# Performance work log

Measured on AMD Instinct MI355X. Metric: run time of the kernel, lower is better.

## Reference

```python
import jax, jax.numpy as jnp
import numpy as np

PART = 0  # index of '<PART>' tag in vocab (select_part_tag = zeros)
W = 3     # max_word_len


def lstm_scan(x_seq, h0, c0, Wih, Whh, bih, bhh):
    """x_seq: [S, N, D] -> outputs [S, N, H]. torch LSTM gate order i, f, g, o."""
    def cell(carry, x):
        h, c = carry
        g = x @ Wih.T + bih + h @ Whh.T + bhh
        i, f, gg, o = jnp.split(g, 4, axis=-1)
        c = jax.nn.sigmoid(f) * c + jax.nn.sigmoid(i) * jnp.tanh(gg)
        h = jax.nn.sigmoid(o) * jnp.tanh(c)
        return (h, c), h
    _, hs = jax.lax.scan(cell, (h0, c0), x_seq)
    return hs


def decoder_probs(win, h0, emb, Wih, Whh, bih, bhh, Wp, bp):
    """Decoder.forward for all start positions at once.
    win: [N, W] candidate-word tokens; h0: [N, H] (used as both h0 and c0).
    Returns [W, N]: row y = log p(word win[:, :y+1] then <PART>)."""
    N = win.shape[0]
    toks = jnp.concatenate([jnp.full((N, 1), PART, win.dtype), win], axis=1)  # prepend <PART>
    x = jnp.swapaxes(emb[toks], 0, 1)                    # [W+1, N, D]
    hs = lstm_scan(x, h0, h0, Wih, Whh, bih, bhh)        # [W+1, N, H]
    logits = hs @ Wp.T + bp                              # [W+1, N, V]
    logZ = jax.nn.logsumexp(logits, axis=-1)             # [W+1, N]
    # log_softmax gathered at target char / <PART> tag positions
    char = jnp.take_along_axis(logits[:-1], win.T[:, :, None], axis=-1)[..., 0] - logZ[:-1]  # [W, N]
    tag = logits[1:, :, PART] - logZ[1:]                 # [W, N]
    return jnp.cumsum(char, axis=0) + tag                # cumulative char logprob + end tag


def forward_loss(sentence, emb, enc, decf, decb):
    B, T = sentence.shape
    H = enc[1].shape[1]
    fvec = sentence
    bvec = jnp.flip(sentence, axis=1)

    def encode(vec):
        toks = jnp.concatenate([jnp.full((B, 1), PART, vec.dtype), vec[:, :-1]], axis=1)
        x = jnp.swapaxes(emb[toks], 0, 1)                # [T, B, D]
        z = jnp.zeros((B, H), emb.dtype)
        return lstm_scan(x, z, z, *enc)                  # [T, B, H]

    enc_f, enc_b = encode(fvec), encode(bvec)
    idx = jnp.clip(jnp.arange(T)[:, None] + jnp.arange(W)[None, :], 0, T - 1)  # [T, W]

    def run_dec(vec, enc_out, params):
        win = vec[:, idx].reshape(B * T, W)              # window starting at each position
        h0 = jnp.swapaxes(enc_out, 0, 1).reshape(B * T, -1)
        p = decoder_probs(win, h0, emb, *params)         # [W, B*T]
        return p.reshape(W, B, T).transpose(2, 0, 1)     # [T(start), W(len-1), B]

    fwdP = run_dec(fvec, enc_f, decf)
    bwdP = run_dec(bvec, enc_b, decb)

    xs = jnp.arange(T)[:, None]
    ys = jnp.arange(W)[None, :]
    # SGB_A.add_bidirection: P[x, y, b] = score of word of length y+1 ending at position x
    P = 0.5 * (fwdP[jnp.clip(xs - ys, 0, T - 1), ys] + bwdP[T - 1 - xs, ys])  # [T, W, B]

    # compute_all_probability: semi-CRF forward recursion
    NEG = jnp.asarray(-1e30, P.dtype)
    def step(buf, inp):
        # buf[i] = total[j-1-i]
        p_j, j = inp
        cand = jnp.where((jnp.arange(W) < j)[:, None], buf + p_j, NEG)
        tot = jax.nn.logsumexp(cand, axis=0)
        return jnp.concatenate([tot[None], buf[:-1]], axis=0), tot

    _, totals = jax.lax.scan(step, jnp.zeros((W, B), P.dtype), (P, jnp.arange(1, T + 1)))
    return -jnp.mean(totals[-1])


def setup_inputs() -> dict:
    key = jax.random.key(0)
    V, D, H, B, T = 8000, 256, 256, 16, 128
    ks = jax.random.split(key, 24)
    s_d = 1.0 / np.sqrt(D)
    s_h = 1.0 / np.sqrt(H)

    def mat(k, shape, scale):
        return jax.random.normal(k, shape, jnp.float32) * scale

    def lstm_p(k):
        k1, k2, k3, k4 = jax.random.split(k, 4)
        return (mat(k1, (4 * H, D), s_d), mat(k2, (4 * H, H), s_h),
                mat(k3, (4 * H,), s_h), mat(k4, (4 * H,), s_h))

    enc = lstm_p(ks[1])
    decf_l = lstm_p(ks[2])
    decb_l = lstm_p(ks[3])
    inp = {
        "sentence": jax.random.randint(ks[0], (B, T), 0, V, jnp.int32),
        "emb": mat(ks[4], (V, D), 1.0),
        "enc_Wih": enc[0], "enc_Whh": enc[1], "enc_bih": enc[2], "enc_bhh": enc[3],
        "decf_Wih": decf_l[0], "decf_Whh": decf_l[1], "decf_bih": decf_l[2], "decf_bhh": decf_l[3],
        "decf_Wp": mat(ks[5], (V, H), s_h), "decf_bp": mat(ks[6], (V,), s_h),
        "decb_Wih": decb_l[0], "decb_Whh": decb_l[1], "decb_bih": decb_l[2], "decb_bhh": decb_l[3],
        "decb_Wp": mat(ks[7], (V, H), s_h), "decb_bp": mat(ks[8], (V,), s_h),
    }
    return inp


def reference(sentence, emb, enc_Wih, enc_Whh, enc_bih, enc_bhh,
              decf_Wih, decf_Whh, decf_bih, decf_bhh, decf_Wp, decf_bp,
              decb_Wih, decb_Whh, decb_bih, decb_bhh, decb_Wp, decb_bp):
    return forward_loss(
        sentence, emb,
        (enc_Wih, enc_Whh, enc_bih, enc_bhh),
        (decf_Wih, decf_Whh, decf_bih, decf_bhh, decf_Wp, decf_bp),
        (decb_Wih, decb_Whh, decb_bih, decb_bhh, decb_Wp, decb_bp))
```

## Files before the change

### kernel.cpp

```cpp
#include <hip/hip_runtime.h>
#include <math.h>

#define VOCAB 8000
#define NN 2048

typedef unsigned short u16;
typedef __attribute__((ext_vector_type(8))) short short8v;
typedef __attribute__((ext_vector_type(4))) short short4v;
typedef __attribute__((ext_vector_type(4))) float float4v;
typedef __attribute__((ext_vector_type(4))) int int4v;

#define OFF_WPBF   0ul
#define OFF_WDEC   2048000ul
#define OFF_XENC   2572288ul
#define OFF_H0BF   4153344ul
#define OFF_DECX   4677632ul
#define OFF_CDEC   6250496ul
#define OFF_HSBF   7299072ul
#define OFF_GBUF   9396224ul
#define OFF_LOGZ   13590528ul
#define OFF_GCH    13606912ul
#define OFF_GTG    13619200ul
#define OFF_P      13631488ul
#define OFF_WTOK   13637632ul
#define OFF_XP0    13649920ul
#define OFF_ENCW   13652032ul
#define OFF_SENC   13914240ul
#define OFF_SQ     13915264ul
#define OFF_WQI8   13916288ul

__device__ __forceinline__ float sigf(float x) { return 1.0f / (1.0f + __expf(-x)); }
__device__ __forceinline__ float tanhsafe(float x) {
    x = fminf(15.0f, fmaxf(-15.0f, x));
    float e = __expf(2.0f * x);
    return (e - 1.0f) / (e + 1.0f);
}
__device__ __forceinline__ u16 f2bf(float f) {
    union { float f; unsigned int u; } x; x.f = f;
    return (u16)((x.u + 0x7fffu + ((x.u >> 16) & 1u)) >> 16);
}
__device__ __forceinline__ float bf2f(u16 x) {
    union { unsigned int u; float f; } v; v.u = ((unsigned int)x) << 16;
    return v.f;
}

__device__ __forceinline__ short8v ldfrag(const u16* lds, int row, int k, int lane, int SB) {
    int r = row + (lane & 15);
    int off = r * SB + ((k + ((lane >> 4) << 3)) << 1);
    off ^= (r & 7) << 4;
    return *(const short8v*)((const char*)lds + off);
}

__device__ __forceinline__ void stage128x256(const u16* __restrict__ g, int row0, int rowmax,
                                             int rowstride, int col0, u16* lds, int tid) {
    #pragma unroll
    for (int it = 0; it < 16; ++it) {
        int chunk = tid + it * 256;
        int r = chunk >> 5;
        int kc = (chunk & 31) << 3;
        short8v v = {0, 0, 0, 0, 0, 0, 0, 0};
        if (row0 + r < rowmax)
            v = *(const short8v*)(g + (size_t)(row0 + r) * rowstride + col0 + kc);
        int off = (r * 512 + kc * 2) ^ ((r & 7) << 4);
        *(short8v*)((char*)lds + off) = v;
    }
}


__global__ __launch_bounds__(256) void k_wpbf(const float* __restrict__ Wf,
                                              const float* __restrict__ Wb,
                                              u16* __restrict__ out) {
    int chunk = blockIdx.x * 256 + threadIdx.x;
    int kc = (chunk & 31) << 3;
    int v = (chunk >> 5) % 8000;
    int d = chunk / (8000 * 32);
    const float* src = (d ? Wb : Wf) + (size_t)v * 256 + kc;
    u16 t8[8];
    #pragma unroll
    for (int j = 0; j < 8; ++j) t8[j] = f2bf(src[j]);
    *(short8v*)(out + ((size_t)d * 8000 + v) * 256 + kc) = *(short8v*)t8;
}

__global__ __launch_bounds__(256) void k_wdecbf(const float* __restrict__ fWhh, const float* __restrict__ fWih,
                                                const float* __restrict__ bWhh, const float* __restrict__ bWih,
                                                u16* __restrict__ out) {
    int chunk = blockIdx.x * 256 + threadIdx.x;
    int kc = (chunk & 63) << 3;
    int r = (chunk >> 6) & 1023;
    int d = chunk >> 16;
    const float* Whh = d ? bWhh : fWhh;
    const float* Wih = d ? bWih : fWih;
    const float* src = (kc < 256) ? (Whh + (size_t)r * 256 + kc) : (Wih + (size_t)r * 256 + (kc - 256));
    u16 t8[8];
    #pragma unroll
    for (int j = 0; j < 8; ++j) t8[j] = f2bf(src[j]);
    *(short8v*)(out + ((size_t)d * 1024 + r) * 512 + kc) = *(short8v*)t8;
}

__global__ __launch_bounds__(256) void k_wencbf(const float* __restrict__ Whh, const float* __restrict__ Wih,
                                                u16* __restrict__ out) {
    int chunk = blockIdx.x * 256 + threadIdx.x;
    int kc = (chunk & 63) << 3;
    int r = chunk >> 6;
    const float* src = (kc < 256) ? (Whh + (size_t)r * 256 + kc) : (Wih + (size_t)r * 256 + (kc - 256));
    u16 t8[8];
    #pragma unroll
    for (int j = 0; j < 8; ++j) t8[j] = f2bf(src[j]);
    *(short8v*)(out + (size_t)r * 512 + kc) = *(short8v*)t8;
}

__global__ __launch_bounds__(256) void k_escale(const float* __restrict__ Whh,
                                                float* __restrict__ s_enc,
                                                float* __restrict__ sq) {
    int r = blockIdx.x * 256 + threadIdx.x;
    if (r >= 1024) return;
    float m = 0.0f;
    for (int k = 0; k < 256; ++k) m = fmaxf(m, fabsf(Whh[r * 256 + k]));
    s_enc[r] = m / 16129.0f;
    sq[r] = (m > 0.0f) ? 127.0f / m : 0.0f;
}

__global__ __launch_bounds__(256) void k_wq2(const float* __restrict__ Whh,
                                             const float* __restrict__ sq,
                                             signed char* __restrict__ wq) {
    int lin = blockIdx.x * 256 + threadIdx.x;
    int lane = lin & 63;
    int ks = (lin >> 6) & 3;
    int c = (lin >> 8) & 3;
    int w = lin >> 10;
    int r = c * 256 + w * 16 + (lane & 15);
    int kb = ks * 64 + ((lane >> 4) << 4);
    float s = sq[r];
    signed char o16[16];
    #pragma unroll
    for (int j = 0; j < 16; ++j) {
        float q = rintf(Whh[r * 256 + kb + j] * s);
        q = fminf(127.0f, fmaxf(-127.0f, q));
        o16[j] = (signed char)q;
    }
    *(int4v*)(wq + (size_t)lin * 16) = *(int4v*)o16;
}

__global__ __launch_bounds__(256) void k_xenc(const int* __restrict__ S, const float* __restrict__ emb,
                                              u16* __restrict__ out) {
    int chunk = blockIdx.x * 256 + threadIdx.x;
    int kc = (chunk & 31) << 3;
    int b = (chunk >> 5) & 15;
    int t = (chunk >> 9) & 127;
    int d = chunk >> 16;
    int tok = 0;
    if (t > 0) tok = d ? S[b * 128 + 128 - t] : S[b * 128 + t - 1];
    const float* src = emb + (size_t)tok * 256 + kc;
    u16 t8[8];
    #pragma unroll
    for (int j = 0; j < 8; ++j) t8[j] = f2bf(src[j]);
    *(short8v*)(out + (size_t)(((d * 128 + t) * 16) + b) * 256 + kc) = *(short8v*)t8;
}

__global__ __launch_bounds__(256) void k_decx(const int* __restrict__ S, const float* __restrict__ emb,
                                              u16* __restrict__ decX, int* __restrict__ winTok) {
    int chunk = blockIdx.x * 256 + threadIdx.x;
    int kc = (chunk & 31) << 3;
    int n = (chunk >> 5) & 2047;
    int r2 = chunk >> 16;
    int s = r2 % 3, d = r2 / 3;
    int b = n >> 7, tq = n & 127;
    int pos = min(tq + s, 127);
    int tok = d ? S[b * 128 + 127 - pos] : S[b * 128 + pos];
    const float* src = emb + (size_t)tok * 256 + kc;
    u16 t8[8];
    #pragma unroll
    for (int j = 0; j < 8; ++j) t8[j] = f2bf(src[j]);
    *(short8v*)(decX + ((size_t)(d * 3 + s) * NN + n) * 256 + kc) = *(short8v*)t8;
    if ((chunk & 31) == 0) winTok[(d * 3 + s) * NN + n] = tok;
}

__global__ __launch_bounds__(256) void k_xp0(const float* __restrict__ emb,
                                             const float* __restrict__ Wihf,
                                             const float* __restrict__ Wihb,
                                             float* __restrict__ xp0) {
    int idx = blockIdx.x * 256 + threadIdx.x;
    int d = idx >> 10, r = idx & 1023;
    const float* Wih = d ? Wihb : Wihf;
    float acc = 0.0f;
    for (int k = 0; k < 256; ++k) acc = fmaf(emb[k], Wih[r * 256 + k], acc);
    xp0[idx] = acc;
}

__global__ __launch_bounds__(256) void k_xproj(const u16* __restrict__ xEncBF,
                                               const u16* __restrict__ encW,
                                               const float* __restrict__ ebih,
                                               const float* __restrict__ ebhh,
                                               float* __restrict__ xpT) {
    __shared__ u16 At[128 * 256];
    __shared__ u16 Bt[128 * 256];
    const int tid = threadIdx.x, lane = tid & 63, wid = tid >> 6;
    const int wm = wid >> 1, wv = wid & 1;
    const int r0 = blockIdx.x * 128, n0 = blockIdx.y * 128, d = blockIdx.z;
    stage128x256(xEncBF + (size_t)d * 2048 * 256, n0, 1 << 30, 256, 0, At, tid);
    stage128x256(encW, r0, 1 << 30, 512, 256, Bt, tid);
    __syncthreads();
    float4v acc[4][4];
    #pragma unroll
    for (int m = 0; m < 4; ++m)
        #pragma unroll
        for (int v = 0; v < 4; ++v) acc[m][v] = (float4v){0.f, 0.f, 0.f, 0.f};
    #pragma unroll
    for (int k = 0; k < 8; ++k) {
        short8v af[4], bf[4];
        #pragma unroll
        for (int m = 0; m < 4; ++m) af[m] = ldfrag(At, wm * 64 + m * 16, k * 32, lane, 512);
        #pragma unroll
        for (int v = 0; v < 4; ++v) bf[v] = ldfrag(Bt, wv * 64 + v * 16, k * 32, lane, 512);
        #pragma unroll
        for (int m = 0; m < 4; ++m)
            #pragma unroll
            for (int v = 0; v < 4; ++v)
                acc[m][v] = __builtin_amdgcn_mfma_f32_16x16x32_bf16(af[m], bf[v], acc[m][v], 0, 0, 0);
    }
    float bs[4]; int rg[4];
    #pragma unroll
    for (int v = 0; v < 4; ++v) {
        rg[v] = r0 + wv * 64 + v * 16 + (lane & 15);
        bs[v] = ebih[rg[v]] + ebhh[rg[v]];
    }
    #pragma unroll
    for (int m = 0; m < 4; ++m)
        #pragma unroll
        for (int i = 0; i < 4; ++i) {
            int n = n0 + wm * 64 + m * 16 + ((lane >> 4) << 2) + i;
            int t_ = n >> 4, bfull = n & 15;
            #pragma unroll
            for (int v = 0; v < 4; ++v) {
                int g = rg[v] >> 8, u = rg[v] & 255;
                size_t idx4 = (((size_t)(d * 16 + bfull) * 128 + t_) * 16 + (u >> 4)) * 16 + (u & 15);
                xpT[idx4 * 4 + g] = acc[m][v][i] + bs[v];
            }
        }
}

__global__ __launch_bounds__(1024) void k_enc5(const signed char* __restrict__ wq,
                                               const float* __restrict__ s_enc,
                                               const float4v* __restrict__ xpT4,
                                               u16* __restrict__ h0bf) {
    __shared__ signed char hbuf[2][4096];
    const int tid = threadIdx.x, lane = tid & 63, w = tid >> 6;
    const int blk = blockIdx.x, d = blk >> 4, b = blk & 15;
    const int l15 = lane & 15, hi = lane >> 4;
    int4v breg[4][4];
    #pragma unroll
    for (int c = 0; c < 4; ++c)
        #pragma unroll
        for (int ks = 0; ks < 4; ++ks)
            breg[c][ks] = *(const int4v*)(wq + ((size_t)(((w * 4 + c) * 4 + ks) * 64 + lane)) * 16);
    float sreg[4];
    #pragma unroll
    for (int c = 0; c < 4; ++c) sreg[c] = s_enc[c * 256 + w * 16 + l15];
    float creg = 0.0f;
    ((long*)hbuf)[tid] = 0l;
    const bool cellane = (lane < 16);
    const int u = w * 16 + l15;
    const float4v* xbase = xpT4 + ((size_t)(d * 16 + b) * 128) * 256 + w * 16 + l15;
    float4v xv_next = {0.f, 0.f, 0.f, 0.f};
    if (cellane) xv_next = xbase[0];
    __syncthreads();
    for (int t = 0; t < 128; ++t) {
        int cur = t & 1;
        float4v xv = xv_next;
        if (cellane && t < 127) xv_next = xbase[(size_t)(t + 1) * 256];
        int4v af[4];
        #pragma unroll
        for (int ks = 0; ks < 4; ++ks) {
            int off = (l15 * 256 + ks * 64 + hi * 16) ^ ((l15 & 7) << 4);
            af[ks] = *(const int4v*)(hbuf[cur] + off);
        }
        int4v acc[4];
        #pragma unroll
        for (int c = 0; c < 4; ++c) {
            acc[c] = (int4v){0, 0, 0, 0};
            #pragma unroll
            for (int ks = 0; ks < 4; ++ks)
                acc[c] = __builtin_amdgcn_mfma_i32_16x16x64_i8(af[ks], breg[c][ks], acc[c], 0, 0, 0);
        }
        if (cellane) {
            float gi = (float)acc[0][0] * sreg[0] + xv[0];
            float gf = (float)acc[1][0] * sreg[1] + xv[1];
            float gG = (float)acc[2][0] * sreg[2] + xv[2];
            float go = (float)acc[3][0] * sreg[3] + xv[3];
            float cn = sigf(gf) * creg + sigf(gi) * tanhsafe(gG);
            float h = sigf(go) * tanhsafe(cn);
            creg = cn;
            h0bf[((size_t)d * NN + b * 128 + t) * 256 + u] = f2bf(h);
            hbuf[cur ^ 1][u] = (signed char)rintf(h * 127.0f);
        }
        __syncthreads();
    }
}

__global__ __launch_bounds__(256) void k_decmm(const u16* __restrict__ Ah, size_t ahStride,
                                               const u16* __restrict__ Axx, size_t axStride,
                                               const u16* __restrict__ Wdec,
                                               const float* __restrict__ bihf, const float* __restrict__ bhhf,
                                               const float* __restrict__ bihb, const float* __restrict__ bhhb,
                                               const float* __restrict__ xp0, int useX,
                                               float* __restrict__ gBuf) {
    __shared__ u16 At[128 * 256];
    __shared__ u16 Bt[128 * 256];
    const int tid = threadIdx.x, lane = tid & 63, wid = tid >> 6;
    const int wm = wid >> 1, wv = wid & 1;
    const int r0 = blockIdx.x * 128, n0 = blockIdx.y * 128, d = blockIdx.z;
    float4v acc[4][4];
    #pragma unroll
    for (int m = 0; m < 4; ++m)
        #pragma unroll
        for (int v = 0; v < 4; ++v) acc[m][v] = (float4v){0.f, 0.f, 0.f, 0.f};
    const int nph = useX ? 2 : 1;
    for (int ph = 0; ph < nph; ++ph) {
        const u16* Asrc = (ph == 0) ? (Ah + (size_t)d * ahStride) : (Axx + (size_t)d * axStride);
        stage128x256(Asrc, n0, 1 << 30, 256, 0, At, tid);
        stage128x256(Wdec + (size_t)d * 1024 * 512, r0, 1 << 30, 512, ph * 256, Bt, tid);
        __syncthreads();
        #pragma unroll
        for (int k = 0; k < 8; ++k) {
            short8v af[4], bf[4];
            #pragma unroll
            for (int m = 0; m < 4; ++m) af[m] = ldfrag(At, wm * 64 + m * 16, k * 32, lane, 512);
            #pragma unroll
            for (int v = 0; v < 4; ++v) bf[v] = ldfrag(Bt, wv * 64 + v * 16, k * 32, lane, 512);
            #pragma unroll
            for (int m = 0; m < 4; ++m)
                #pragma unroll
                for (int v = 0; v < 4; ++v)
                    acc[m][v] = __builtin_amdgcn_mfma_f32_16x16x32_bf16(af[m], bf[v], acc[m][v], 0, 0, 0);
        }
        __syncthreads();
    }
    const float* bih = d ? bihb : bihf;
    const float* bhh = d ? bhhb : bhhf;
    float bs[4]; int rg[4];
    #pragma unroll
    for (int v = 0; v < 4; ++v) {
        rg[v] = r0 + wv * 64 + v * 16 + (lane & 15);
        bs[v] = bih[rg[v]] + bhh[rg[v]];
        if (!useX) bs[v] += xp0[d * 1024 + rg[v]];
    }
    #pragma unroll
    for (int m = 0; m < 4; ++m)
        #pragma unroll
        for (int i = 0; i < 4; ++i) {
            int n = n0 + wm * 64 + m * 16 + ((lane >> 4) << 2) + i;
            #pragma unroll
            for (int v = 0; v < 4; ++v)
                gBuf[((size_t)d * NN + n) * 1024 + rg[v]] = acc[m][v][i] + bs[v];
        }
}

__global__ __launch_bounds__(256) void k_deccell(const float* __restrict__ gBuf,
                                                 const u16* __restrict__ h0bf,
                                                 float* __restrict__ cDec,
                                                 u16* __restrict__ hsBF, int s) {
    int flat = blockIdx.x * 256 + threadIdx.x;
    int j = flat & 255;
    int n = (flat >> 8) & 2047;
    int d = flat >> 19;
    const float* g = gBuf + ((size_t)d * NN + n) * 1024;
    float gi = g[j], gf = g[j + 256], gg = g[j + 512], go = g[j + 768];
    float cprev = (s == 0) ? bf2f(h0bf[flat]) : cDec[flat];
    float cn = sigf(gf) * cprev + sigf(gi) * tanhsafe(gg);
    float h = sigf(go) * tanhsafe(cn);
    cDec[flat] = cn;
    hsBF[((size_t)(d * 4 + s) * NN + n) * 256 + j] = f2bf(h);
}

__global__ __launch_bounds__(512, 2) void k_proj8(const u16* __restrict__ hsBF,
                                                  const u16* __restrict__ WpBF,
                                                  const float* __restrict__ bpf, const float* __restrict__ bpb,
                                                  const int* __restrict__ winTok,
                                                  float* __restrict__ partials,
                                                  float* __restrict__ gchar, float* __restrict__ gtag) {
    __shared__ u16 At[128 * 256];
    __shared__ u16 Bt[2][64 * 256];
    const int tid = threadIdx.x, lane = tid & 63, w = tid >> 6;
    const int wm = w >> 1, wv = w & 1;
    const int l15 = lane & 15, hi = lane >> 4;
    const int L = blockIdx.x;
    const int chunkI = L & 7, idx = L >> 3;
    const int n0 = (idx & 15) * 128, d = idx >> 4;
    const int vt0 = chunkI * 16;
    const int nvt = min(16, 125 - vt0);
    const float* bp = d ? bpb : bpf;

#define LOADB8(vt_) do {                                                          \
        _Pragma("unroll")                                                         \
        for (int it = 0; it < 4; ++it) {                                          \
            int g = tid + it * 512; int r = g >> 5, kc = (g & 31) << 3;           \
            bregs[it] = *(const short8v*)(WpBF + ((size_t)d * 8000 + (vt_) * 64 + r) * 256 + kc); \
        }                                                                         \
    } while (0)
#define WRITEB8(buf_) do {                                                        \
        _Pragma("unroll")                                                         \
        for (int it = 0; it < 4; ++it) {                                          \
            int g = tid + it * 512; int r = g >> 5, kc = (g & 31) << 3;           \
            int off = (r * 512 + kc * 2) ^ ((r & 7) << 4);                        \
            *(short8v*)((char*)Bt[buf_] + off) = bregs[it];                       \
        }                                                                         \
    } while (0)

    short8v bregs[4];
    for (int s = 0; s < 4; ++s) {
        const u16* hsA = hsBF + (size_t)(d * 4 + s) * NN * 256;
        #pragma unroll
        for (int it = 0; it < 8; ++it) {
            int chunk = tid + it * 512;
            int r = chunk >> 5, kc = (chunk & 31) << 3;
            short8v v8 = *(const short8v*)(hsA + (size_t)(n0 + r) * 256 + kc);
            int off = (r * 512 + kc * 2) ^ ((r & 7) << 4);
            *(short8v*)((char*)At + off) = v8;
        }
        LOADB8(vt0);
        WRITEB8(0);
        int tok[2][4];
        #pragma unroll
        for (int m = 0; m < 2; ++m)
            #pragma unroll
            for (int i = 0; i < 4; ++i) {
                int n = n0 + wm * 32 + m * 16 + hi * 4 + i;
                tok[m][i] = (s < 3) ? winTok[(d * 3 + s) * NN + n] : -1;
            }
        float expsum[2][4] = {{0.f, 0.f, 0.f, 0.f}, {0.f, 0.f, 0.f, 0.f}};
        __syncthreads();
        short8v afr[2][8];
        #pragma unroll
        for (int m = 0; m < 2; ++m)
            #pragma unroll
            for (int kk = 0; kk < 8; ++kk) {
                afr[m][kk] = ldfrag(At, wm * 32 + m * 16, kk * 32, lane, 512);
                asm volatile("" : "+v"(afr[m][kk]));
            }
        int cur = 0;
        for (int t = 0; t < nvt; ++t) {
            int vt = vt0 + t;
            if (t + 1 < nvt) LOADB8(vt + 1);
            float bpv[2];
            #pragma unroll
            for (int v = 0; v < 2; ++v) bpv[v] = bp[vt * 64 + wv * 32 + v * 16 + l15];
            float4v acc[2][2];
            #pragma unroll
            for (int m = 0; m < 2; ++m)
                #pragma unroll
                for (int v = 0; v < 2; ++v) acc[m][v] = (float4v){0.f, 0.f, 0.f, 0.f};
            #pragma unroll
            for (int kk = 0; kk < 8; ++kk) {
                short8v bf[2];
                #pragma unroll
                for (int v = 0; v < 2; ++v) bf[v] = ldfrag(Bt[cur], wv * 32 + v * 16, kk * 32, lane, 512);
                #pragma unroll
                for (int m = 0; m < 2; ++m)
                    #pragma unroll
                    for (int v = 0; v < 2; ++v)
                        acc[m][v] = __builtin_amdgcn_mfma_f32_16x16x32_bf16(afr[m][kk], bf[v], acc[m][v], 0, 0, 0);
            }
            #pragma unroll
            for (int m = 0; m < 2; ++m)
                #pragma unroll
                for (int i = 0; i < 4; ++i) {
                    int n = n0 + wm * 32 + m * 16 + hi * 4 + i;
                    float es = 0.0f;
                    #pragma unroll
                    for (int v = 0; v < 2; ++v) {
                        int vgv = vt * 64 + wv * 32 + v * 16 + l15;
                        float lg = acc[m][v][i] + bpv[v];
                        es += __expf(lg);
                        if (vgv == tok[m][i]) gchar[(d * 3 + s) * NN + n] = lg;
                        if (s >= 1 && vgv == 0) gtag[(d * 3 + (s - 1)) * NN + n] = lg;
                    }
                    expsum[m][i] += es;
                }
            __syncthreads();
            if (t + 1 < nvt) WRITEB8(cur ^ 1);
            __syncthreads();
            cur ^= 1;
        }
        #pragma unroll
        for (int m = 0; m < 2; ++m)
            #pragma unroll
            for (int i = 0; i < 4; ++i) {
                float e = expsum[m][i];
                #pragma unroll
                for (int off = 1; off <= 8; off <<= 1) e += __shfl_xor(e, off);
                if (l15 == 0) {
                    int n = n0 + wm * 32 + m * 16 + hi * 4 + i;
                    partials[((size_t)(d * 4 + s) * NN + n) * 16 + chunkI * 2 + wv] = e;
                }
            }
    }
#undef LOADB8
#undef WRITEB8
}

__global__ __launch_bounds__(256) void k_lzsum(const float* __restrict__ partials,
                                               float* __restrict__ logZ) {
    int row = blockIdx.x * 256 + threadIdx.x;
    const float* p = partials + (size_t)row * 16;
    float s = 0.0f;
    #pragma unroll
    for (int c = 0; c < 16; ++c) s += p[c];
    logZ[row] = __logf(s);
}

__global__ __launch_bounds__(256) void k_passm(const float* __restrict__ gchar,
                                               const float* __restrict__ gtag,
                                               const float* __restrict__ logZ,
                                               float* __restrict__ P) {
    int flat = blockIdx.x * 256 + threadIdx.x;
    if (flat >= 128 * 3 * 16) return;
    int b = flat & 15;
    int y = (flat >> 4) % 3;
    int x = flat / 48;
    int nf = b * 128 + min(127, max(0, x - y));
    int nb = b * 128 + 127 - x;
    float pf = 0.0f, pb = 0.0f;
    for (int ss = 0; ss <= y; ++ss) {
        pf += gchar[ss * NN + nf] - logZ[ss * NN + nf];
        pb += gchar[(3 + ss) * NN + nb] - logZ[(4 + ss) * NN + nb];
    }
    pf += gtag[y * NN + nf] - logZ[(y + 1) * NN + nf];
    pb += gtag[(3 + y) * NN + nb] - logZ[(4 + y + 1) * NN + nb];
    P[flat] = 0.5f * (pf + pb);
}

__global__ __launch_bounds__(64) void k_scan(const float* __restrict__ P, float* __restrict__ out) {
    __shared__ float Pl[128 * 48];
    int tid = threadIdx.x;
    #pragma unroll
    for (int it = 0; it < 96; ++it) Pl[tid + it * 64] = P[tid + it * 64];
    __syncthreads();
    if (tid < 16) {
        int b = tid;
        float b0 = 0.f, b1 = 0.f, b2 = 0.f, tot = 0.f;
        for (int j = 1; j <= 128; ++j) {
            float c0 = b0 + Pl[((j - 1) * 3 + 0) * 16 + b];
            float c1 = (j >= 2) ? b1 + Pl[((j - 1) * 3 + 1) * 16 + b] : -1e30f;
            float c2 = (j >= 3) ? b2 + Pl[((j - 1) * 3 + 2) * 16 + b] : -1e30f;
            float mx = fmaxf(c0, fmaxf(c1, c2));
            float sv = __expf(c0 - mx) + __expf(c1 - mx) + __expf(c2 - mx);
            tot = mx + __logf(sv);
            b2 = b1; b1 = b0; b0 = tot;
        }
        #pragma unroll
        for (int off = 1; off <= 8; off <<= 1) tot += __shfl_xor(tot, off);
        if (b == 0) out[0] = -tot / 16.0f;
    }
}

extern "C" void kernel_launch(void* const* d_in, const int* in_sizes, int n_in,
                              void* d_out, int out_size, void* d_ws, size_t ws_size,
                              hipStream_t stream) {
    const int* S = (const int*)d_in[0];
    const float* emb = (const float*)d_in[1];
    const float* eWih = (const float*)d_in[2];
    const float* eWhh = (const float*)d_in[3];
    const float* ebih = (const float*)d_in[4];
    const float* ebhh = (const float*)d_in[5];
    const float* fWih = (const float*)d_in[6];
    const float* fWhh = (const float*)d_in[7];
    const float* fbih = (const float*)d_in[8];
    const float* fbhh = (const float*)d_in[9];
    const float* fWp  = (const float*)d_in[10];
    const float* fbp  = (const float*)d_in[11];
    const float* bWih = (const float*)d_in[12];
    const float* bWhh = (const float*)d_in[13];
    const float* bbih = (const float*)d_in[14];
    const float* bbhh = (const float*)d_in[15];
    const float* bWp  = (const float*)d_in[16];
    const float* bbp  = (const float*)d_in[17];

    float* w = (float*)d_ws;
    u16* WpBF    = (u16*)(w + OFF_WPBF);
    u16* WdecBF  = (u16*)(w + OFF_WDEC);
    u16* xEncBF  = (u16*)(w + OFF_XENC);
    u16* h0bf    = (u16*)(w + OFF_H0BF);
    u16* decXBF  = (u16*)(w + OFF_DECX);
    float* cDec  = w + OFF_CDEC;
    u16* hsBF    = (u16*)(w + OFF_HSBF);
    float* gBuf  = w + OFF_GBUF;
    float* xpT   = gBuf;
    float* partials = gBuf;
    float* logZ  = w + OFF_LOGZ;
    float* gchar = w + OFF_GCH;
    float* gtag  = w + OFF_GTG;
    float* Pm    = w + OFF_P;
    int* winTok  = (int*)(w + OFF_WTOK);
    float* xp0   = w + OFF_XP0;
    u16* encW    = (u16*)(w + OFF_ENCW);
    float* sEnc  = w + OFF_SENC;
    float* sQ    = w + OFF_SQ;
    signed char* wqEnc = (signed char*)(w + OFF_WQI8);

    k_wpbf<<<2000, 256, 0, stream>>>(fWp, bWp, WpBF);
    k_wdecbf<<<512, 256, 0, stream>>>(fWhh, fWih, bWhh, bWih, WdecBF);
    k_wencbf<<<256, 256, 0, stream>>>(eWhh, eWih, encW);
    k_escale<<<4, 256, 0, stream>>>(eWhh, sEnc, sQ);
    k_wq2<<<64, 256, 0, stream>>>(eWhh, sQ, wqEnc);
    k_xenc<<<512, 256, 0, stream>>>(S, emb, xEncBF);
    k_decx<<<1536, 256, 0, stream>>>(S, emb, decXBF, winTok);
    k_xp0<<<8, 256, 0, stream>>>(emb, fWih, bWih, xp0);

    k_xproj<<<dim3(8, 16, 2), 256, 0, stream>>>(xEncBF, encW, ebih, ebhh, xpT);
    k_enc5<<<32, 1024, 0, stream>>>(wqEnc, sEnc, (const float4v*)xpT, h0bf);

    for (int s = 0; s < 4; ++s) {
        const u16* Ah; size_t ahS;
        const u16* Axx; size_t axS;
        if (s == 0) {
            Ah = h0bf; ahS = (size_t)NN * 256;
            Axx = decXBF; axS = (size_t)3 * NN * 256;
        } else {
            Ah = hsBF + (size_t)(s - 1) * NN * 256; ahS = (size_t)4 * NN * 256;
            Axx = decXBF + (size_t)(s - 1) * NN * 256; axS = (size_t)3 * NN * 256;
        }
        k_decmm<<<dim3(8, 16, 2), 256, 0, stream>>>(Ah, ahS, Axx, axS, WdecBF,
                                                    fbih, fbhh, bbih, bbhh, xp0,
                                                    (s == 0) ? 0 : 1, gBuf);
        k_deccell<<<4096, 256, 0, stream>>>(gBuf, h0bf, cDec, hsBF, s);
    }

    k_proj8<<<256, 512, 0, stream>>>(hsBF, WpBF, fbp, bbp, winTok,
                                     partials, gchar, gtag);
    k_lzsum<<<64, 256, 0, stream>>>(partials, logZ);
    k_passm<<<24, 256, 0, stream>>>(gchar, gtag, logZ, Pm);
    k_scan<<<1, 64, 0, stream>>>(Pm, (float*)d_out);
}
```

Before: 492.6 us.

## Overlap decoder input projection with encoder recurrence and merge setup kernels

```diff
diff --git a/kernel.cpp b/kernel.cpp
--- a/kernel.cpp
+++ b/kernel.cpp
@@ -28,6 +28,8 @@
 #define OFF_SENC   13914240ul
 #define OFF_SQ     13915264ul
 #define OFF_WQI8   13916288ul
+#define OFF_GXD    13981824ul
+#define WS_NEED_OV ((OFF_GXD + 6291456ul) * 4ul)
 
 __device__ __forceinline__ float sigf(float x) { return 1.0f / (1.0f + __expf(-x)); }
 __device__ __forceinline__ float tanhsafe(float x) {
@@ -66,125 +68,110 @@
     }
 }
 
-
-__global__ __launch_bounds__(256) void k_wpbf(const float* __restrict__ Wf,
-                                              const float* __restrict__ Wb,
-                                              u16* __restrict__ out) {
-    int chunk = blockIdx.x * 256 + threadIdx.x;
-    int kc = (chunk & 31) << 3;
-    int v = (chunk >> 5) % 8000;
-    int d = chunk / (8000 * 32);
-    const float* src = (d ? Wb : Wf) + (size_t)v * 256 + kc;
-    u16 t8[8];
-    #pragma unroll
-    for (int j = 0; j < 8; ++j) t8[j] = f2bf(src[j]);
-    *(short8v*)(out + ((size_t)d * 8000 + v) * 256 + kc) = *(short8v*)t8;
-}
-
-__global__ __launch_bounds__(256) void k_wdecbf(const float* __restrict__ fWhh, const float* __restrict__ fWih,
-                                                const float* __restrict__ bWhh, const float* __restrict__ bWih,
-                                                u16* __restrict__ out) {
-    int chunk = blockIdx.x * 256 + threadIdx.x;
-    int kc = (chunk & 63) << 3;
-    int r = (chunk >> 6) & 1023;
-    int d = chunk >> 16;
-    const float* Whh = d ? bWhh : fWhh;
-    const float* Wih = d ? bWih : fWih;
-    const float* src = (kc < 256) ? (Whh + (size_t)r * 256 + kc) : (Wih + (size_t)r * 256 + (kc - 256));
-    u16 t8[8];
-    #pragma unroll
-    for (int j = 0; j < 8; ++j) t8[j] = f2bf(src[j]);
-    *(short8v*)(out + ((size_t)d * 1024 + r) * 512 + kc) = *(short8v*)t8;
-}
-
-__global__ __launch_bounds__(256) void k_wencbf(const float* __restrict__ Whh, const float* __restrict__ Wih,
-                                                u16* __restrict__ out) {
-    int chunk = blockIdx.x * 256 + threadIdx.x;
-    int kc = (chunk & 63) << 3;
-    int r = chunk >> 6;
-    const float* src = (kc < 256) ? (Whh + (size_t)r * 256 + kc) : (Wih + (size_t)r * 256 + (kc - 256));
-    u16 t8[8];
-    #pragma unroll
-    for (int j = 0; j < 8; ++j) t8[j] = f2bf(src[j]);
-    *(short8v*)(out + (size_t)r * 512 + kc) = *(short8v*)t8;
-}
-
-__global__ __launch_bounds__(256) void k_escale(const float* __restrict__ Whh,
-                                                float* __restrict__ s_enc,
-                                                float* __restrict__ sq) {
-    int r = blockIdx.x * 256 + threadIdx.x;
-    if (r >= 1024) return;
-    float m = 0.0f;
-    for (int k = 0; k < 256; ++k) m = fmaxf(m, fabsf(Whh[r * 256 + k]));
-    s_enc[r] = m / 16129.0f;
-    sq[r] = (m > 0.0f) ? 127.0f / m : 0.0f;
-}
-
-__global__ __launch_bounds__(256) void k_wq2(const float* __restrict__ Whh,
-                                             const float* __restrict__ sq,
-                                             signed char* __restrict__ wq) {
-    int lin = blockIdx.x * 256 + threadIdx.x;
-    int lane = lin & 63;
-    int ks = (lin >> 6) & 3;
-    int c = (lin >> 8) & 3;
-    int w = lin >> 10;
-    int r = c * 256 + w * 16 + (lane & 15);
-    int kb = ks * 64 + ((lane >> 4) << 4);
-    float s = sq[r];
-    signed char o16[16];
-    #pragma unroll
-    for (int j = 0; j < 16; ++j) {
-        float q = rintf(Whh[r * 256 + kb + j] * s);
-        q = fminf(127.0f, fmaxf(-127.0f, q));
-        o16[j] = (signed char)q;
-    }
-    *(int4v*)(wq + (size_t)lin * 16) = *(int4v*)o16;
-}
-
-__global__ __launch_bounds__(256) void k_xenc(const int* __restrict__ S, const float* __restrict__ emb,
-                                              u16* __restrict__ out) {
-    int chunk = blockIdx.x * 256 + threadIdx.x;
-    int kc = (chunk & 31) << 3;
-    int b = (chunk >> 5) & 15;
-    int t = (chunk >> 9) & 127;
-    int d = chunk >> 16;
-    int tok = 0;
-    if (t > 0) tok = d ? S[b * 128 + 128 - t] : S[b * 128 + t - 1];
-    const float* src = emb + (size_t)tok * 256 + kc;
-    u16 t8[8];
-    #pragma unroll
-    for (int j = 0; j < 8; ++j) t8[j] = f2bf(src[j]);
-    *(short8v*)(out + (size_t)(((d * 128 + t) * 16) + b) * 256 + kc) = *(short8v*)t8;
-}
-
-__global__ __launch_bounds__(256) void k_decx(const int* __restrict__ S, const float* __restrict__ emb,
-                                              u16* __restrict__ decX, int* __restrict__ winTok) {
-    int chunk = blockIdx.x * 256 + threadIdx.x;
-    int kc = (chunk & 31) << 3;
-    int n = (chunk >> 5) & 2047;
-    int r2 = chunk >> 16;
-    int s = r2 % 3, d = r2 / 3;
-    int b = n >> 7, tq = n & 127;
-    int pos = min(tq + s, 127);
-    int tok = d ? S[b * 128 + 127 - pos] : S[b * 128 + pos];
-    const float* src = emb + (size_t)tok * 256 + kc;
-    u16 t8[8];
-    #pragma unroll
-    for (int j = 0; j < 8; ++j) t8[j] = f2bf(src[j]);
-    *(short8v*)(decX + ((size_t)(d * 3 + s) * NN + n) * 256 + kc) = *(short8v*)t8;
-    if ((chunk & 31) == 0) winTok[(d * 3 + s) * NN + n] = tok;
-}
-
-__global__ __launch_bounds__(256) void k_xp0(const float* __restrict__ emb,
-                                             const float* __restrict__ Wihf,
-                                             const float* __restrict__ Wihb,
-                                             float* __restrict__ xp0) {
-    int idx = blockIdx.x * 256 + threadIdx.x;
-    int d = idx >> 10, r = idx & 1023;
-    const float* Wih = d ? Wihb : Wihf;
-    float acc = 0.0f;
-    for (int k = 0; k < 256; ++k) acc = fmaf(emb[k], Wih[r * 256 + k], acc);
-    xp0[idx] = acc;
+__global__ __launch_bounds__(256) void k_setup(const int* __restrict__ S,
+                                               const float* __restrict__ emb,
+                                               const float* __restrict__ eWih, const float* __restrict__ eWhh,
+                                               const float* __restrict__ fWih, const float* __restrict__ fWhh,
+                                               const float* __restrict__ fWp,
+                                               const float* __restrict__ bWih, const float* __restrict__ bWhh,
+                                               const float* __restrict__ bWp,
+                                               u16* __restrict__ WpBF, u16* __restrict__ WdecBF,
+                                               u16* __restrict__ encW,
+                                               float* __restrict__ s_enc, signed char* __restrict__ wq,
+                                               u16* __restrict__ xEncBF,
+                                               u16* __restrict__ decX, int* __restrict__ winTok,
+                                               float* __restrict__ xp0) {
+    const int b = blockIdx.x, tid = threadIdx.x;
+    if (b < 2000) {
+        int chunk = b * 256 + tid;
+        int kc = (chunk & 31) << 3;
+        int v = (chunk >> 5) % 8000;
+        int d = chunk / (8000 * 32);
+        const float* src = (d ? bWp : fWp) + (size_t)v * 256 + kc;
+        u16 t8[8];
+        #pragma unroll
+        for (int j = 0; j < 8; ++j) t8[j] = f2bf(src[j]);
+        *(short8v*)(WpBF + ((size_t)d * 8000 + v) * 256 + kc) = *(short8v*)t8;
+    } else if (b < 2512) {
+        int chunk = (b - 2000) * 256 + tid;
+        int kc = (chunk & 63) << 3;
+        int r = (chunk >> 6) & 1023;
+        int d = chunk >> 16;
+        const float* Whh = d ? bWhh : fWhh;
+        const float* Wih = d ? bWih : fWih;
+        const float* src = (kc < 256) ? (Whh + (size_t)r * 256 + kc) : (Wih + (size_t)r * 256 + (kc - 256));
+        u16 t8[8];
+        #pragma unroll
+        for (int j = 0; j < 8; ++j) t8[j] = f2bf(src[j]);
+        *(short8v*)(WdecBF + ((size_t)d * 1024 + r) * 512 + kc) = *(short8v*)t8;
+    } else if (b < 2768) {
+        int chunk = (b - 2512) * 256 + tid;
+        int kc = (chunk & 63) << 3;
+        int r = chunk >> 6;
+        const float* src = (kc < 256) ? (eWhh + (size_t)r * 256 + kc) : (eWih + (size_t)r * 256 + (kc - 256));
+        u16 t8[8];
+        #pragma unroll
+        for (int j = 0; j < 8; ++j) t8[j] = f2bf(src[j]);
+        *(short8v*)(encW + (size_t)r * 512 + kc) = *(short8v*)t8;
+    } else if (b < 2832) {
+        int lin = (b - 2768) * 256 + tid;
+        int lane = lin & 63;
+        int ks = (lin >> 6) & 3;
+        int c = (lin >> 8) & 3;
+        int w = lin >> 10;
+        int r = c * 256 + w * 16 + (lane & 15);
+        float m = 0.0f;
+        for (int k = 0; k < 256; k += 4) {
+            float4 v4 = *(const float4*)(eWhh + (size_t)r * 256 + k);
+            m = fmaxf(m, fmaxf(fmaxf(fabsf(v4.x), fabsf(v4.y)), fmaxf(fabsf(v4.z), fabsf(v4.w))));
+        }
+        float sqv = (m > 0.0f) ? 127.0f / m : 0.0f;
+        if (ks == 0 && lane < 16) s_enc[r] = m / 16129.0f;
+        int kb = ks * 64 + ((lane >> 4) << 4);
+        signed char o16[16];
+        #pragma unroll
+        for (int j = 0; j < 16; ++j) {
+            float q = rintf(eWhh[(size_t)r * 256 + kb + j] * sqv);
+            q = fminf(127.0f, fmaxf(-127.0f, q));
+            o16[j] = (signed char)q;
+        }
+        *(int4v*)(wq + (size_t)lin * 16) = *(int4v*)o16;
+    } else if (b < 3344) {
+        int chunk = (b - 2832) * 256 + tid;
+        int kc = (chunk & 31) << 3;
+        int bb = (chunk >> 5) & 15;
+        int t = (chunk >> 9) & 127;
+        int d = chunk >> 16;
+        int tok = 0;
+        if (t > 0) tok = d ? S[bb * 128 + 128 - t] : S[bb * 128 + t - 1];
+        const float* src = emb + (size_t)tok * 256 + kc;
+        u16 t8[8];
+        #pragma unroll
+        for (int j = 0; j < 8; ++j) t8[j] = f2bf(src[j]);
+        *(short8v*)(xEncBF + (size_t)(((d * 128 + t) * 16) + bb) * 256 + kc) = *(short8v*)t8;
+    } else if (b < 4880) {
+        int chunk = (b - 3344) * 256 + tid;
+        int kc = (chunk & 31) << 3;
+        int n = (chunk >> 5) & 2047;
+        int r2 = chunk >> 16;
+        int s = r2 % 3, d = r2 / 3;
+        int bb = n >> 7, tq = n & 127;
+        int pos = min(tq + s, 127);
+        int tok = d ? S[bb * 128 + 127 - pos] : S[bb * 128 + pos];
+        const float* src = emb + (size_t)tok * 256 + kc;
+        u16 t8[8];
+        #pragma unroll
+        for (int j = 0; j < 8; ++j) t8[j] = f2bf(src[j]);
+        *(short8v*)(decX + ((size_t)(d * 3 + s) * NN + n) * 256 + kc) = *(short8v*)t8;
+        if ((chunk & 31) == 0) winTok[(d * 3 + s) * NN + n] = tok;
+    } else {
+        int idx = (b - 4880) * 256 + tid;
+        int d = idx >> 10, r = idx & 1023;
+        const float* Wih = d ? bWih : fWih;
+        float acc = 0.0f;
+        for (int k = 0; k < 256; ++k) acc = fmaf(emb[k], Wih[r * 256 + k], acc);
+        xp0[idx] = acc;
+    }
 }
 
 __global__ __launch_bounds__(256) void k_xproj(const u16* __restrict__ xEncBF,
@@ -239,61 +226,122 @@
         }
 }
 
-__global__ __launch_bounds__(1024) void k_enc5(const signed char* __restrict__ wq,
+__global__ __launch_bounds__(1024) void k_encx(const signed char* __restrict__ wq,
                                                const float* __restrict__ s_enc,
                                                const float4v* __restrict__ xpT4,
-                                               u16* __restrict__ h0bf) {
-    __shared__ signed char hbuf[2][4096];
+                                               u16* __restrict__ h0bf,
+                                               const u16* __restrict__ decXBF,
+                                               const u16* __restrict__ WdecBF,
+                                               const float* __restrict__ fbih, const float* __restrict__ fbhh,
+                                               const float* __restrict__ bbih, const float* __restrict__ bbhh,
+                                               u16* __restrict__ gXdec) {
+    __shared__ char smem[131072];
     const int tid = threadIdx.x, lane = tid & 63, w = tid >> 6;
-    const int blk = blockIdx.x, d = blk >> 4, b = blk & 15;
     const int l15 = lane & 15, hi = lane >> 4;
-    int4v breg[4][4];
-    #pragma unroll
-    for (int c = 0; c < 4; ++c)
-        #pragma unroll
-        for (int ks = 0; ks < 4; ++ks)
-            breg[c][ks] = *(const int4v*)(wq + ((size_t)(((w * 4 + c) * 4 + ks) * 64 + lane)) * 16);
-    float sreg[4];
-    #pragma unroll
-    for (int c = 0; c < 4; ++c) sreg[c] = s_enc[c * 256 + w * 16 + l15];
-    float creg = 0.0f;
-    ((long*)hbuf)[tid] = 0l;
-    const bool cellane = (lane < 16);
-    const int u = w * 16 + l15;
-    const float4v* xbase = xpT4 + ((size_t)(d * 16 + b) * 128) * 256 + w * 16 + l15;
-    float4v xv_next = {0.f, 0.f, 0.f, 0.f};
-    if (cellane) xv_next = xbase[0];
-    __syncthreads();
-    for (int t = 0; t < 128; ++t) {
-        int cur = t & 1;
-        float4v xv = xv_next;
-        if (cellane && t < 127) xv_next = xbase[(size_t)(t + 1) * 256];
-        int4v af[4];
-        #pragma unroll
-        for (int ks = 0; ks < 4; ++ks) {
-            int off = (l15 * 256 + ks * 64 + hi * 16) ^ ((l15 & 7) << 4);
-            af[ks] = *(const int4v*)(hbuf[cur] + off);
-        }
-        int4v acc[4];
-        #pragma unroll
-        for (int c = 0; c < 4; ++c) {
-            acc[c] = (int4v){0, 0, 0, 0};
+    if (blockIdx.x < 32) {
+        signed char (*hbuf)[4096] = (signed char(*)[4096])smem;
+        const int blk = blockIdx.x, d = blk >> 4, b = blk & 15;
+        int4v breg[4][4];
+        #pragma unroll
+        for (int c = 0; c < 4; ++c)
             #pragma unroll
             for (int ks = 0; ks < 4; ++ks)
-                acc[c] = __builtin_amdgcn_mfma_i32_16x16x64_i8(af[ks], breg[c][ks], acc[c], 0, 0, 0);
-        }
-        if (cellane) {
-            float gi = (float)acc[0][0] * sreg[0] + xv[0];
-            float gf = (float)acc[1][0] * sreg[1] + xv[1];
-            float gG = (float)acc[2][0] * sreg[2] + xv[2];
-            float go = (float)acc[3][0] * sreg[3] + xv[3];
-            float cn = sigf(gf) * creg + sigf(gi) * tanhsafe(gG);
-            float h = sigf(go) * tanhsafe(cn);
-            creg = cn;
-            h0bf[((size_t)d * NN + b * 128 + t) * 256 + u] = f2bf(h);
-            hbuf[cur ^ 1][u] = (signed char)rintf(h * 127.0f);
-        }
+                breg[c][ks] = *(const int4v*)(wq + ((size_t)(((w * 4 + c) * 4 + ks) * 64 + lane)) * 16);
+        float sreg[4];
+        #pragma unroll
+        for (int c = 0; c < 4; ++c) sreg[c] = s_enc[c * 256 + w * 16 + l15];
+        float creg = 0.0f;
+        ((long*)hbuf)[tid & 1023] = 0l;
+        const bool cellane = (lane < 16);
+        const int u = w * 16 + l15;
+        const float4v* xbase = xpT4 + ((size_t)(d * 16 + b) * 128) * 256 + w * 16 + l15;
+        float4v xv_next = {0.f, 0.f, 0.f, 0.f};
+        if (cellane) xv_next = xbase[0];
         __syncthreads();
+        for (int t = 0; t < 128; ++t) {
+            int cur = t & 1;
+            float4v xv = xv_next;
+            if (cellane && t < 127) xv_next = xbase[(size_t)(t + 1) * 256];
+            int4v af[4];
+            #pragma unroll
+            for (int ks = 0; ks < 4; ++ks) {
+                int off = (l15 * 256 + ks * 64 + hi * 16) ^ ((l15 & 7) << 4);
+                af[ks] = *(const int4v*)(hbuf[cur] + off);
+            }
+            int4v acc[4];
+            #pragma unroll
+            for (int c = 0; c < 4; ++c) {
+                acc[c] = (int4v){0, 0, 0, 0};
+                #pragma unroll
+                for (int ks = 0; ks < 4; ++ks)
+                    acc[c] = __builtin_amdgcn_mfma_i32_16x16x64_i8(af[ks], breg[c][ks], acc[c], 0, 0, 0);
+            }
+            if (cellane) {
+                float gi = (float)acc[0][0] * sreg[0] + xv[0];
+                float gf = (float)acc[1][0] * sreg[1] + xv[1];
+                float gG = (float)acc[2][0] * sreg[2] + xv[2];
+                float go = (float)acc[3][0] * sreg[3] + xv[3];
+                float cn = sigf(gf) * creg + sigf(gi) * tanhsafe(gG);
+                float h = sigf(go) * tanhsafe(cn);
+                creg = cn;
+                h0bf[((size_t)d * NN + b * 128 + t) * 256 + u] = f2bf(h);
+                hbuf[cur ^ 1][u] = (signed char)rintf(h * 127.0f);
+            }
+            __syncthreads();
+        }
+    } else {
+        u16* At = (u16*)smem;
+        u16* Bt = (u16*)(smem + 65536);
+        const int bi = blockIdx.x - 32;
+        const int rt = bi & 7, nt = (bi >> 3) & 15, rest = bi >> 7;
+        const int sx = rest % 3, d = rest / 3;
+        const int r0 = rt * 128, n0 = nt * 128;
+        const int wm = w >> 2, wv = w & 3;
+        const u16* Asrc = decXBF + (size_t)(d * 3 + sx) * NN * 256;
+        const u16* Bsrc = WdecBF + (size_t)d * 1024 * 512;
+        #pragma unroll
+        for (int it = 0; it < 4; ++it) {
+            int chunk = tid + it * 1024;
+            int r = chunk >> 5, kc = (chunk & 31) << 3;
+            short8v va = *(const short8v*)(Asrc + (size_t)(n0 + r) * 256 + kc);
+            short8v vb = *(const short8v*)(Bsrc + (size_t)(r0 + r) * 512 + 256 + kc);
+            int off = (r * 512 + kc * 2) ^ ((r & 7) << 4);
+            *(short8v*)((char*)At + off) = va;
+            *(short8v*)((char*)Bt + off) = vb;
+        }
+        __syncthreads();
+        float4v acc[2][2];
+        #pragma unroll
+        for (int m = 0; m < 2; ++m)
+            #pragma unroll
+            for (int v = 0; v < 2; ++v) acc[m][v] = (float4v){0.f, 0.f, 0.f, 0.f};
+        #pragma unroll
+        for (int kk = 0; kk < 8; ++kk) {
+            short8v af[2], bf[2];
+            #pragma unroll
+            for (int m = 0; m < 2; ++m) af[m] = ldfrag(At, wm * 32 + m * 16, kk * 32, lane, 512);
+            #pragma unroll
+            for (int v = 0; v < 2; ++v) bf[v] = ldfrag(Bt, wv * 32 + v * 16, kk * 32, lane, 512);
+            #pragma unroll
+            for (int m = 0; m < 2; ++m)
+                #pragma unroll
+                for (int v = 0; v < 2; ++v)
+                    acc[m][v] = __builtin_amdgcn_mfma_f32_16x16x32_bf16(af[m], bf[v], acc[m][v], 0, 0, 0);
+        }
+        const float* bih = d ? bbih : fbih;
+        const float* bhh = d ? bbhh : fbhh;
+        #pragma unroll
+        for (int m = 0; m < 2; ++m)
+            #pragma unroll
+            for (int i = 0; i < 4; ++i) {
+                int n = n0 + wm * 32 + m * 16 + hi * 4 + i;
+                #pragma unroll
+                for (int v = 0; v < 2; ++v) {
+                    int r = r0 + wv * 32 + v * 16 + l15;
+                    float val = acc[m][v][i] + bih[r] + bhh[r];
+                    gXdec[((size_t)(d * 3 + sx) * NN + n) * 1024 + r] = f2bf(val);
+                }
+            }
     }
 }
 
@@ -302,7 +350,8 @@
                                                const u16* __restrict__ Wdec,
                                                const float* __restrict__ bihf, const float* __restrict__ bhhf,
                                                const float* __restrict__ bihb, const float* __restrict__ bhhb,
-                                               const float* __restrict__ xp0, int useX,
+                                               const float* __restrict__ xp0, int s,
+                                               const u16* __restrict__ gXdec,
                                                float* __restrict__ gBuf) {
     __shared__ u16 At[128 * 256];
     __shared__ u16 Bt[128 * 256];
@@ -314,7 +363,8 @@
     for (int m = 0; m < 4; ++m)
         #pragma unroll
         for (int v = 0; v < 4; ++v) acc[m][v] = (float4v){0.f, 0.f, 0.f, 0.f};
-    const int nph = useX ? 2 : 1;
+    const int useX = (s >= 1);
+    const int nph = (useX && !gXdec) ? 2 : 1;
     for (int ph = 0; ph < nph; ++ph) {
         const u16* Asrc = (ph == 0) ? (Ah + (size_t)d * ahStride) : (Axx + (size_t)d * axStride);
         stage128x256(Asrc, n0, 1 << 30, 256, 0, At, tid);
@@ -337,12 +387,13 @@
     }
     const float* bih = d ? bihb : bihf;
     const float* bhh = d ? bhhb : bhhf;
-    float bs[4]; int rg[4];
+    int rg[4];
+    float bs[4] = {0.f, 0.f, 0.f, 0.f};
     #pragma unroll
     for (int v = 0; v < 4; ++v) {
         rg[v] = r0 + wv * 64 + v * 16 + (lane & 15);
-        bs[v] = bih[rg[v]] + bhh[rg[v]];
-        if (!useX) bs[v] += xp0[d * 1024 + rg[v]];
+        if (!useX) bs[v] = bih[rg[v]] + bhh[rg[v]] + xp0[d * 1024 + rg[v]];
+        else if (!gXdec) bs[v] = bih[rg[v]] + bhh[rg[v]];
     }
     #pragma unroll
     for (int m = 0; m < 4; ++m)
@@ -350,8 +401,12 @@
         for (int i = 0; i < 4; ++i) {
             int n = n0 + wm * 64 + m * 16 + ((lane >> 4) << 2) + i;
             #pragma unroll
-            for (int v = 0; v < 4; ++v)
-                gBuf[((size_t)d * NN + n) * 1024 + rg[v]] = acc[m][v][i] + bs[v];
+            for (int v = 0; v < 4; ++v) {
+                float g = acc[m][v][i] + bs[v];
+                if (useX && gXdec)
+                    g += bf2f(gXdec[((size_t)(d * 3 + s - 1) * NN + n) * 1024 + rg[v]]);
+                gBuf[((size_t)d * NN + n) * 1024 + rg[v]] = g;
+            }
         }
 }
 
@@ -594,21 +649,23 @@
     float* xp0   = w + OFF_XP0;
     u16* encW    = (u16*)(w + OFF_ENCW);
     float* sEnc  = w + OFF_SENC;
-    float* sQ    = w + OFF_SQ;
     signed char* wqEnc = (signed char*)(w + OFF_WQI8);
-
-    k_wpbf<<<2000, 256, 0, stream>>>(fWp, bWp, WpBF);
-    k_wdecbf<<<512, 256, 0, stream>>>(fWhh, fWih, bWhh, bWih, WdecBF);
-    k_wencbf<<<256, 256, 0, stream>>>(eWhh, eWih, encW);
-    k_escale<<<4, 256, 0, stream>>>(eWhh, sEnc, sQ);
-    k_wq2<<<64, 256, 0, stream>>>(eWhh, sQ, wqEnc);
-    k_xenc<<<512, 256, 0, stream>>>(S, emb, xEncBF);
-    k_decx<<<1536, 256, 0, stream>>>(S, emb, decXBF, winTok);
-    k_xp0<<<8, 256, 0, stream>>>(emb, fWih, bWih, xp0);
+    u16* gXdec   = (u16*)(w + OFF_GXD);
+
+    const bool useOv = (ws_size >= WS_NEED_OV);
+
+    k_setup<<<4888, 256, 0, stream>>>(S, emb, eWih, eWhh, fWih, fWhh, fWp,
+                                      bWih, bWhh, bWp,
+                                      WpBF, WdecBF, encW, sEnc, wqEnc,
+                                      xEncBF, decXBF, winTok, xp0);
 
     k_xproj<<<dim3(8, 16, 2), 256, 0, stream>>>(xEncBF, encW, ebih, ebhh, xpT);
-    k_enc5<<<32, 1024, 0, stream>>>(wqEnc, sEnc, (const float4v*)xpT, h0bf);
-
+
+    k_encx<<<useOv ? 800 : 32, 1024, 0, stream>>>(wqEnc, sEnc, (const float4v*)xpT, h0bf,
+                                                  decXBF, WdecBF, fbih, fbhh, bbih, bbhh,
+                                                  gXdec);
+
+    const u16* gx = useOv ? gXdec : nullptr;
     for (int s = 0; s < 4; ++s) {
         const u16* Ah; size_t ahS;
         const u16* Axx; size_t axS;
@@ -621,7 +678,7 @@
         }
         k_decmm<<<dim3(8, 16, 2), 256, 0, stream>>>(Ah, ahS, Axx, axS, WdecBF,
                                                     fbih, fbhh, bbih, bbhh, xp0,
-                                                    (s == 0) ? 0 : 1, gBuf);
+                                                    s, gx, gBuf);
         k_deccell<<<4096, 256, 0, stream>>>(gBuf, h0bf, cDec, hsBF, s);
     }
 
```

Measured after the change: 473.3 us. -3.9%, faster.
